# Kernel tuning notes

Hardware: AMD Instinct MI355X
Metric: run time of the kernel (lower is better)

The kernel has to match this reference:

```python
import math
import jax, jax.numpy as jnp
import numpy as np

B, H, D, N, M = 4, 8, 64, 8192, 256
EPS = 1e-6


def sample_orthogonal_random_vectors(num_rows, num_cols, seed=0):
    """Faithful port of FavorAttention.sample_orthogonal_random_vectors."""
    rng = np.random.default_rng(seed)
    num_blocks = math.ceil(num_rows / num_cols)
    unstructured = rng.standard_normal((num_blocks, num_cols, num_cols)).astype(np.float32)
    norm = np.linalg.norm(unstructured, axis=-1).reshape(-1, 1)
    q, _ = np.linalg.qr(unstructured)                 # reduced QR per block
    q = np.transpose(q, (0, 2, 1)).reshape(-1, num_cols)
    q = q[:num_rows, :] * norm[:num_rows, :]
    return jnp.asarray(q, dtype=jnp.float32)


def setup_inputs() -> dict:
    key = jax.random.key(0)
    kq, kk, kv = jax.random.split(key, 3)
    return {
        "query": jax.random.normal(kq, (B, H, D, N), dtype=jnp.float32),
        "key": jax.random.normal(kk, (B, H, D, N), dtype=jnp.float32),
        "value": jax.random.normal(kv, (B, H, D, N), dtype=jnp.float32),
        "projection_matrix": sample_orthogonal_random_vectors(M, D),
    }


def randomized_kernel(x, proj, is_query, eps=EPS):
    """FAVOR+ positive softmax features. x: [B,H,D,N] -> phi: [B,H,M,N]."""
    d = x.shape[2]
    data_normalizer = d ** -0.25
    ratio = proj.shape[0] ** -0.5
    # projected: [B,H,M,N]
    u = jnp.einsum('md,bhdn->bhmn', proj, x) * data_normalizer
    # ||x||^2 / (2*sqrt(d)) per token: [B,H,1,N]
    diag = jnp.sum(x * x, axis=2, keepdims=True) * (data_normalizer ** 2) * 0.5
    if is_query:
        stab = jnp.max(u, axis=2, keepdims=True)            # per-token max over features
    else:
        stab = jnp.max(u, axis=(2, 3), keepdims=True)       # global max per (b,h)
    return ratio * (jnp.exp(u - diag - stab) + eps)


def reference(query, key, value, projection_matrix):
    q_phi = randomized_kernel(query, projection_matrix, is_query=True)    # [B,H,M,N]
    k_phi = randomized_kernel(key, projection_matrix, is_query=False)     # [B,H,M,N]
    # kv = key @ value^T over sequence: [B,H,M,D]
    kv = jnp.einsum('bhmn,bhdn->bhmd', k_phi, value)
    key_norm = jnp.sum(k_phi, axis=3)                                     # [B,H,M]
    out = jnp.einsum('bhmn,bhmd->bhnd', q_phi, kv)                        # [B,H,N,D]
    out_norm = jnp.einsum('bhmn,bhm->bhn', q_phi, key_norm)[..., None]    # [B,H,N,1]
    out = out / out_norm
    return jnp.swapaxes(out, 2, 3)                                        # [B,H,D,N]


if __name__ == '__main__':
    o = reference(**setup_inputs())
    print(o.shape, o.dtype)
```

## Files before the change

### kernel.cpp

```cpp
#include <hip/hip_runtime.h>


typedef short s16x8 __attribute__((ext_vector_type(8)));
typedef float f32x4 __attribute__((ext_vector_type(4)));

#define Dv 64
#define Nv 8192
#define Mv 256
#define BHv 32
#define SPL 16
#define NSPL (Nv / SPL)
#define NCH (NSPL / 64)

#define DNRM 0.3535533905932738f
#define EPSV 1e-6f
#define KSTAB 15.0f

#define OFF_KVA 0
#define OFF_KNA (OFF_KVA + BHv * Mv * Dv)
#define OFF_SVA (OFF_KNA + BHv * Mv)
#define OFF_SGM (OFF_SVA + BHv * Dv)
#define OFF_KNF (OFF_SGM + BHv * 64)
#define OFF_KVT (OFF_KNF + BHv * Mv)
#define ZERO_FLOATS (OFF_SVA + BHv * Dv)

__device__ __forceinline__ unsigned short f2b(float x) {
    return __builtin_bit_cast(unsigned short, (__bf16)x);
}

__device__ __forceinline__ s16x8 load_pfrag(const float* __restrict__ proj, int m,
                                            int kc, int q) {
    const float* p = proj + m * 64 + kc * 32 + q * 8;
    s16x8 r;
#pragma unroll
    for (int j = 0; j < 8; ++j) r[j] = (short)f2b(p[j]);
    return r;
}

__global__ __launch_bounds__(256, 2) void favor_kv(const float* __restrict__ key,
                                                   const float* __restrict__ value,
                                                   const float* __restrict__ proj,
                                                   float* __restrict__ ws) {
    __shared__ __align__(16) unsigned short KT[64][72];
    __shared__ __align__(16) unsigned short VL[64][72];
    __shared__ __align__(16) unsigned short PH[256][40];
    __shared__ __align__(16) float dred[16][64];
    __shared__ __align__(16) float dgl[64];
    const int tid = threadIdx.x;
    const int w = tid >> 6, l = tid & 63, c = l & 15, q = l >> 4;
    const int g = tid >> 4, cs = tid & 15;
    const int s = blockIdx.x, bh = blockIdx.y;
    const float* kp = key + (size_t)bh * Dv * Nv;
    const float* vp = value + (size_t)bh * Dv * Nv;

    s16x8 P[4][2];
#pragma unroll
    for (int mt = 0; mt < 4; ++mt)
#pragma unroll
        for (int kc = 0; kc < 2; ++kc)
            P[mt][kc] = load_pfrag(proj, (4 * w + mt) * 16 + c, kc, q);

    f32x4 kva[4][4];
#pragma unroll
    for (int mt = 0; mt < 4; ++mt)
#pragma unroll
        for (int dt = 0; dt < 4; ++dt) kva[mt][dt] = (f32x4){0.f, 0.f, 0.f, 0.f};
    float kn[4] = {0.f, 0.f, 0.f, 0.f};
    float sv[4] = {0.f, 0.f, 0.f, 0.f};
    float tmax = -3.0e38f;

    for (int ch = 0; ch < NCH; ++ch) {
        const int n0 = s * NSPL + ch * 64;
        if (ch) __syncthreads();
        {
            float4 kk[4], vv[4];
#pragma unroll
            for (int di = 0; di < 4; ++di) {
                kk[di] = *(const float4*)&kp[(4 * g + di) * Nv + n0 + 4 * cs];
                vv[di] = *(const float4*)&vp[(4 * g + di) * Nv + n0 + 4 * cs];
            }
#pragma unroll
            for (int j = 0; j < 4; ++j) {
                const float k0 = ((const float*)&kk[0])[j];
                const float k1 = ((const float*)&kk[1])[j];
                const float k2 = ((const float*)&kk[2])[j];
                const float k3 = ((const float*)&kk[3])[j];
                *(short4*)&KT[4 * cs + j][4 * g] =
                    make_short4((short)f2b(k0), (short)f2b(k1), (short)f2b(k2),
                                (short)f2b(k3));
                dred[g][4 * cs + j] = (k0 * k0 + k1 * k1) + (k2 * k2 + k3 * k3);
            }
#pragma unroll
            for (int di = 0; di < 4; ++di) {
                *(short4*)&VL[4 * g + di][4 * cs] = make_short4(
                    (short)f2b(vv[di].x), (short)f2b(vv[di].y),
                    (short)f2b(vv[di].z), (short)f2b(vv[di].w));
                sv[di] += (vv[di].x + vv[di].y) + (vv[di].z + vv[di].w);
            }
        }
        __syncthreads();
        if (tid < 64) {
            float ds = 0.f;
#pragma unroll
            for (int gg = 0; gg < 16; ++gg) ds += dred[gg][tid];
            dgl[tid] = ds * 0.0625f;
        }
        __syncthreads();
#pragma unroll
        for (int h = 0; h < 2; ++h) {
#pragma unroll
            for (int nt2 = 0; nt2 < 2; ++nt2) {
                const int nt = 2 * h + nt2;
                const s16x8 a0 = *(const s16x8*)&KT[nt * 16 + c][q * 8];
                const s16x8 a1 = *(const s16x8*)&KT[nt * 16 + c][32 + q * 8];
                const float4 dg = *(const float4*)&dgl[nt * 16 + q * 4];
#pragma unroll
                for (int mt = 0; mt < 4; ++mt) {
                    f32x4 u = {0.f, 0.f, 0.f, 0.f};
                    u = __builtin_amdgcn_mfma_f32_16x16x32_bf16(a0, P[mt][0], u, 0, 0, 0);
                    u = __builtin_amdgcn_mfma_f32_16x16x32_bf16(a1, P[mt][1], u, 0, 0, 0);
                    tmax = fmaxf(tmax, fmaxf(fmaxf(u[0], u[1]), fmaxf(u[2], u[3])));
                    const float e0 = __expf(u[0] * DNRM - dg.x - KSTAB);
                    const float e1 = __expf(u[1] * DNRM - dg.y - KSTAB);
                    const float e2 = __expf(u[2] * DNRM - dg.z - KSTAB);
                    const float e3 = __expf(u[3] * DNRM - dg.w - KSTAB);
                    kn[mt] += (e0 + e1) + (e2 + e3);
                    *(short4*)&PH[(4 * w + mt) * 16 + c][nt2 * 16 + q * 4] =
                        make_short4((short)f2b(e0), (short)f2b(e1),
                                    (short)f2b(e2), (short)f2b(e3));
                }
            }
            s16x8 bf[4];
#pragma unroll
            for (int dt = 0; dt < 4; ++dt)
                bf[dt] = *(const s16x8*)&VL[dt * 16 + c][h * 32 + q * 8];
#pragma unroll
            for (int mt = 0; mt < 4; ++mt) {
                const s16x8 a = *(const s16x8*)&PH[(4 * w + mt) * 16 + c][q * 8];
#pragma unroll
                for (int dt = 0; dt < 4; ++dt)
                    kva[mt][dt] = __builtin_amdgcn_mfma_f32_16x16x32_bf16(
                        a, bf[dt], kva[mt][dt], 0, 0, 0);
            }
        }
    }
#pragma unroll
    for (int off = 1; off < 64; off <<= 1)
        tmax = fmaxf(tmax, __shfl_xor(tmax, off, 64));
    if (l == 0) ws[OFF_SGM + bh * 64 + s * 4 + w] = tmax * DNRM;
    float* kvp = ws + OFF_KVA + (size_t)bh * Mv * Dv;
#pragma unroll
    for (int mt = 0; mt < 4; ++mt) {
        const int mrow = (4 * w + mt) * 16 + 4 * q;
#pragma unroll
        for (int dt = 0; dt < 4; ++dt) {
            const int dcol = dt * 16 + c;
#pragma unroll
            for (int r = 0; r < 4; ++r)
                atomicAdd(&kvp[(size_t)(mrow + r) * Dv + dcol], kva[mt][dt][r]);
        }
    }
#pragma unroll
    for (int mt = 0; mt < 4; ++mt) {
        kn[mt] += __shfl_xor(kn[mt], 16, 64);
        kn[mt] += __shfl_xor(kn[mt], 32, 64);
    }
    if (q == 0) {
#pragma unroll
        for (int mt = 0; mt < 4; ++mt)
            atomicAdd(&ws[OFF_KNA + bh * Mv + (4 * w + mt) * 16 + c], kn[mt]);
    }
    __syncthreads();
    float* sp = &dred[0][0];
#pragma unroll
    for (int di = 0; di < 4; ++di) sp[(4 * g + di) * 16 + cs] = sv[di];
    __syncthreads();
    if (tid < 64) {
        float t2 = 0.f;
#pragma unroll
        for (int j = 0; j < 16; ++j) t2 += sp[tid * 16 + j];
        atomicAdd(&ws[OFF_SVA + bh * 64 + tid], t2);
    }
}

__global__ __launch_bounds__(256) void favor_kvred(float* __restrict__ ws) {
    __shared__ float sAl;
    const int t = threadIdx.x, f = blockIdx.x, bh = blockIdx.y;
    if (t < 64) {
        float v = ws[OFF_SGM + bh * 64 + t];
#pragma unroll
        for (int off = 1; off < 64; off <<= 1)
            v = fmaxf(v, __shfl_xor(v, off, 64));
        if (t == 0) sAl = __expf(KSTAB - v);
    }
    __syncthreads();
    const float al = sAl;
    const int flat = f * 4096 + t * 16;
    const int m = flat >> 6, d0 = flat & 63;
    const float* kva = ws + OFF_KVA + (size_t)bh * Mv * Dv;
    const float* sva = ws + OFF_SVA + bh * 64;
    unsigned short* kvT =
        (unsigned short*)(ws + OFF_KVT) + (size_t)bh * 64 * 256;
    float4 vv[4];
#pragma unroll
    for (int i = 0; i < 4; ++i) vv[i] = *(const float4*)&kva[flat + 4 * i];
#pragma unroll
    for (int i = 0; i < 4; ++i) {
#pragma unroll
        for (int j = 0; j < 4; ++j) {
            const int d = d0 + 4 * i + j;
            const float val = ((const float*)&vv[i])[j] * al + EPSV * sva[d];
            kvT[(size_t)d * 256 + m] = f2b(val);
        }
    }
    if (t < 64) {
        const int mm = f * 64 + t;
        ws[OFF_KNF + bh * Mv + mm] =
            ws[OFF_KNA + bh * Mv + mm] * al + EPSV * (float)Nv;
    }
}

__global__ __launch_bounds__(256, 2) void favor_out(const float* __restrict__ query,
                                                    const float* __restrict__ proj,
                                                    const float* __restrict__ ws,
                                                    float* __restrict__ out) {
    __shared__ __align__(16) unsigned short PHT[64][264];
    __shared__ float npart[4][64];
    __shared__ float knl[256];
    __shared__ float cw[4][64];
    __shared__ float stabl[64];
    __shared__ float dql[64];
    unsigned short (*QT)[72] = (unsigned short (*)[72]) & PHT[0][0];
    float (*dred)[64] = (float (*)[64])((char*)&PHT[0][0] + 9216);
    const int tid = threadIdx.x;
    const int w = tid >> 6, l = tid & 63, c = l & 15, q = l >> 4;
    const int g = tid >> 4, cs = tid & 15;
    const int nb = blockIdx.x, bh = blockIdx.y;
    const int n0 = nb * 64;
    const float* qp = query + (size_t)bh * Dv * Nv;
    const unsigned short* kvT =
        (const unsigned short*)(ws + OFF_KVT) + (size_t)bh * 64 * 256;

    {
        float4 qq[4];
#pragma unroll
        for (int di = 0; di < 4; ++di)
            qq[di] = *(const float4*)&qp[(4 * g + di) * Nv + n0 + 4 * cs];
#pragma unroll
        for (int j = 0; j < 4; ++j) {
            const float v0 = ((const float*)&qq[0])[j];
            const float v1 = ((const float*)&qq[1])[j];
            const float v2 = ((const float*)&qq[2])[j];
            const float v3 = ((const float*)&qq[3])[j];
            *(short4*)&QT[4 * cs + j][4 * g] =
                make_short4((short)f2b(v0), (short)f2b(v1), (short)f2b(v2),
                            (short)f2b(v3));
            dred[g][4 * cs + j] = (v0 * v0 + v1 * v1) + (v2 * v2 + v3 * v3);
        }
    }
    knl[tid] = ws[OFF_KNF + bh * Mv + tid];

    s16x8 P[4][2];
#pragma unroll
    for (int mt = 0; mt < 4; ++mt)
#pragma unroll
        for (int kc = 0; kc < 2; ++kc)
            P[mt][kc] = load_pfrag(proj, (4 * w + mt) * 16 + c, kc, q);
    __syncthreads();

    f32x4 u[4][4];
#pragma unroll
    for (int mt = 0; mt < 4; ++mt)
#pragma unroll
        for (int nt = 0; nt < 4; ++nt) u[mt][nt] = (f32x4){0.f, 0.f, 0.f, 0.f};
#pragma unroll
    for (int nt = 0; nt < 4; ++nt) {
        const s16x8 b0 = *(const s16x8*)&QT[nt * 16 + c][q * 8];
        const s16x8 b1 = *(const s16x8*)&QT[nt * 16 + c][32 + q * 8];
#pragma unroll
        for (int mt = 0; mt < 4; ++mt) {
            u[mt][nt] =
                __builtin_amdgcn_mfma_f32_16x16x32_bf16(P[mt][0], b0, u[mt][nt], 0, 0, 0);
            u[mt][nt] =
                __builtin_amdgcn_mfma_f32_16x16x32_bf16(P[mt][1], b1, u[mt][nt], 0, 0, 0);
        }
    }
#pragma unroll
    for (int nt = 0; nt < 4; ++nt) {
        float vm = -3.4e38f;
#pragma unroll
        for (int mt = 0; mt < 4; ++mt)
            vm = fmaxf(vm, fmaxf(fmaxf(u[mt][nt][0], u[mt][nt][1]),
                                 fmaxf(u[mt][nt][2], u[mt][nt][3])));
        vm = fmaxf(vm, __shfl_xor(vm, 16, 64));
        vm = fmaxf(vm, __shfl_xor(vm, 32, 64));
        if (q == 0) cw[w][nt * 16 + c] = vm;
    }
    __syncthreads();
    if (tid < 64) {
        stabl[tid] =
            fmaxf(fmaxf(cw[0][tid], cw[1][tid]), fmaxf(cw[2][tid], cw[3][tid]));
        float dsum = 0.f;
#pragma unroll
        for (int gg = 0; gg < 16; ++gg) dsum += dred[gg][tid];
        dql[tid] = dsum * 0.0625f;
    }
    __syncthreads();
#pragma unroll
    for (int nt = 0; nt < 4; ++nt) {
        const float sr = stabl[nt * 16 + c];
        const float dq = dql[nt * 16 + c];
        float np = 0.f;
#pragma unroll
        for (int mt = 0; mt < 4; ++mt) {
            const float e0 = __expf((u[mt][nt][0] - sr) * DNRM - dq) + EPSV;
            const float e1 = __expf((u[mt][nt][1] - sr) * DNRM - dq) + EPSV;
            const float e2 = __expf((u[mt][nt][2] - sr) * DNRM - dq) + EPSV;
            const float e3 = __expf((u[mt][nt][3] - sr) * DNRM - dq) + EPSV;
            const int mb = (4 * w + mt) * 16 + 4 * q;
            np += e0 * knl[mb] + e1 * knl[mb + 1] + e2 * knl[mb + 2] +
                  e3 * knl[mb + 3];
            *(short4*)&PHT[nt * 16 + c][mb] = make_short4(
                (short)f2b(e0), (short)f2b(e1), (short)f2b(e2), (short)f2b(e3));
        }
        np += __shfl_xor(np, 16, 64);
        np += __shfl_xor(np, 32, 64);
        if (q == 0) npart[w][nt * 16 + c] = np;
    }
    __syncthreads();
    f32x4 acc[4];
#pragma unroll
    for (int dt = 0; dt < 4; ++dt) acc[dt] = (f32x4){0.f, 0.f, 0.f, 0.f};
#pragma unroll
    for (int kc = 0; kc < 8; ++kc) {
        const s16x8 a = *(const s16x8*)&PHT[w * 16 + c][kc * 32 + q * 8];
#pragma unroll
        for (int dt = 0; dt < 4; ++dt) {
            const s16x8 b =
                *(const s16x8*)&kvT[(size_t)(dt * 16 + c) * 256 + kc * 32 + q * 8];
            acc[dt] = __builtin_amdgcn_mfma_f32_16x16x32_bf16(a, b, acc[dt], 0, 0, 0);
        }
    }
    __syncthreads();
    float* ot = (float*)&PHT[0][0];
    float rn[4];
#pragma unroll
    for (int r = 0; r < 4; ++r) {
        const int nl = w * 16 + 4 * q + r;
        rn[r] = 1.0f / ((npart[0][nl] + npart[1][nl]) +
                        (npart[2][nl] + npart[3][nl]));
    }
#pragma unroll
    for (int dt = 0; dt < 4; ++dt)
#pragma unroll
        for (int r = 0; r < 4; ++r)
            ot[(dt * 16 + c) * 68 + (w * 16 + 4 * q + r)] = acc[dt][r] * rn[r];
    __syncthreads();
    float* op = out + (size_t)bh * Dv * Nv;
    {
        const int d = tid >> 2, ng = (tid & 3) * 16;
#pragma unroll
        for (int i = 0; i < 4; ++i) {
            const float4 v = *(const float4*)&ot[d * 68 + ng + i * 4];
            *(float4*)&op[d * Nv + n0 + ng + i * 4] = v;
        }
    }
}

extern "C" void kernel_launch(void* const* d_in, const int* in_sizes, int n_in,
                              void* d_out, int out_size, void* d_ws, size_t ws_size,
                              hipStream_t stream) {
    const float* q = (const float*)d_in[0];
    const float* k = (const float*)d_in[1];
    const float* v = (const float*)d_in[2];
    const float* proj = (const float*)d_in[3];
    float* ws = (float*)d_ws;
    float* out = (float*)d_out;

    hipMemsetAsync(ws, 0, (size_t)ZERO_FLOATS * sizeof(float), stream);
    favor_kv<<<dim3(SPL, 32), 256, 0, stream>>>(k, v, proj, ws);
    favor_kvred<<<dim3(4, 32), 256, 0, stream>>>(ws);
    favor_out<<<dim3(Nv / 64, 32), 256, 0, stream>>>(q, proj, ws, out);
}
```

Measured before the change: 332.5 us.

## Split favor_kv across 8 waves and replace atomics with per-split partial buffers

The key/value phase now runs 512 threads per block. Half the threads load and convert key, the other half value, and each wave handles 2 feature tiles instead of 4. Global atomicAdd accumulation of kv, key norms and value sums is replaced by per-split partial buffers that favor_kvred reduces, which also removes the workspace memset. The stabilizer constant is folded into the diag term so each exponent needs one FMA. In exchange the workspace grows by 16x for the partial kv buffers, and the reduce kernel reads more data.

```diff
diff --git a/kernel.cpp b/kernel.cpp
--- a/kernel.cpp
+++ b/kernel.cpp
@@ -16,13 +16,12 @@
 #define EPSV 1e-6f
 #define KSTAB 15.0f
 
-#define OFF_KVA 0
-#define OFF_KNA (OFF_KVA + BHv * Mv * Dv)
-#define OFF_SVA (OFF_KNA + BHv * Mv)
-#define OFF_SGM (OFF_SVA + BHv * Dv)
-#define OFF_KNF (OFF_SGM + BHv * 64)
-#define OFF_KVT (OFF_KNF + BHv * Mv)
-#define ZERO_FLOATS (OFF_SVA + BHv * Dv)
+#define OFF_SGM 0
+#define OFF_SVP (OFF_SGM + BHv * SPL * 8)
+#define OFF_KNP (OFF_SVP + BHv * SPL * 64)
+#define OFF_KNF (OFF_KNP + BHv * SPL * Mv)
+#define OFF_KVP (OFF_KNF + BHv * Mv)
+#define OFF_KVT (OFF_KVP + BHv * SPL * Mv * Dv)
 
 __device__ __forceinline__ unsigned short f2b(float x) {
     return __builtin_bit_cast(unsigned short, (__bf16)x);
@@ -37,7 +36,7 @@
     return r;
 }
 
-__global__ __launch_bounds__(256, 2) void favor_kv(const float* __restrict__ key,
+__global__ __launch_bounds__(512, 4) void favor_kv(const float* __restrict__ key,
                                                    const float* __restrict__ value,
                                                    const float* __restrict__ proj,
                                                    float* __restrict__ ws) {
@@ -48,37 +47,36 @@
     __shared__ __align__(16) float dgl[64];
     const int tid = threadIdx.x;
     const int w = tid >> 6, l = tid & 63, c = l & 15, q = l >> 4;
-    const int g = tid >> 4, cs = tid & 15;
+    const int sg = tid >> 4, cs = tid & 15;
     const int s = blockIdx.x, bh = blockIdx.y;
     const float* kp = key + (size_t)bh * Dv * Nv;
     const float* vp = value + (size_t)bh * Dv * Nv;
 
-    s16x8 P[4][2];
-#pragma unroll
-    for (int mt = 0; mt < 4; ++mt)
+    s16x8 P[2][2];
+#pragma unroll
+    for (int mt = 0; mt < 2; ++mt)
 #pragma unroll
         for (int kc = 0; kc < 2; ++kc)
-            P[mt][kc] = load_pfrag(proj, (4 * w + mt) * 16 + c, kc, q);
-
-    f32x4 kva[4][4];
-#pragma unroll
-    for (int mt = 0; mt < 4; ++mt)
+            P[mt][kc] = load_pfrag(proj, (2 * w + mt) * 16 + c, kc, q);
+
+    f32x4 kva[2][4];
+#pragma unroll
+    for (int mt = 0; mt < 2; ++mt)
 #pragma unroll
         for (int dt = 0; dt < 4; ++dt) kva[mt][dt] = (f32x4){0.f, 0.f, 0.f, 0.f};
-    float kn[4] = {0.f, 0.f, 0.f, 0.f};
+    float kn[2] = {0.f, 0.f};
     float sv[4] = {0.f, 0.f, 0.f, 0.f};
     float tmax = -3.0e38f;
 
     for (int ch = 0; ch < NCH; ++ch) {
         const int n0 = s * NSPL + ch * 64;
         if (ch) __syncthreads();
-        {
-            float4 kk[4], vv[4];
-#pragma unroll
-            for (int di = 0; di < 4; ++di) {
+        if (sg < 16) {
+            const int g = sg;
+            float4 kk[4];
+#pragma unroll
+            for (int di = 0; di < 4; ++di)
                 kk[di] = *(const float4*)&kp[(4 * g + di) * Nv + n0 + 4 * cs];
-                vv[di] = *(const float4*)&vp[(4 * g + di) * Nv + n0 + 4 * cs];
-            }
 #pragma unroll
             for (int j = 0; j < 4; ++j) {
                 const float k0 = ((const float*)&kk[0])[j];
@@ -90,9 +88,15 @@
                                 (short)f2b(k3));
                 dred[g][4 * cs + j] = (k0 * k0 + k1 * k1) + (k2 * k2 + k3 * k3);
             }
+        } else {
+            const int g2 = sg - 16;
+            float4 vv[4];
+#pragma unroll
+            for (int di = 0; di < 4; ++di)
+                vv[di] = *(const float4*)&vp[(4 * g2 + di) * Nv + n0 + 4 * cs];
 #pragma unroll
             for (int di = 0; di < 4; ++di) {
-                *(short4*)&VL[4 * g + di][4 * cs] = make_short4(
+                *(short4*)&VL[4 * g2 + di][4 * cs] = make_short4(
                     (short)f2b(vv[di].x), (short)f2b(vv[di].y),
                     (short)f2b(vv[di].z), (short)f2b(vv[di].w));
                 sv[di] += (vv[di].x + vv[di].y) + (vv[di].z + vv[di].w);
@@ -103,7 +107,7 @@
             float ds = 0.f;
 #pragma unroll
             for (int gg = 0; gg < 16; ++gg) ds += dred[gg][tid];
-            dgl[tid] = ds * 0.0625f;
+            dgl[tid] = ds * 0.0625f + KSTAB;
         }
         __syncthreads();
 #pragma unroll
@@ -115,17 +119,17 @@
                 const s16x8 a1 = *(const s16x8*)&KT[nt * 16 + c][32 + q * 8];
                 const float4 dg = *(const float4*)&dgl[nt * 16 + q * 4];
 #pragma unroll
-                for (int mt = 0; mt < 4; ++mt) {
+                for (int mt = 0; mt < 2; ++mt) {
                     f32x4 u = {0.f, 0.f, 0.f, 0.f};
                     u = __builtin_amdgcn_mfma_f32_16x16x32_bf16(a0, P[mt][0], u, 0, 0, 0);
                     u = __builtin_amdgcn_mfma_f32_16x16x32_bf16(a1, P[mt][1], u, 0, 0, 0);
                     tmax = fmaxf(tmax, fmaxf(fmaxf(u[0], u[1]), fmaxf(u[2], u[3])));
-                    const float e0 = __expf(u[0] * DNRM - dg.x - KSTAB);
-                    const float e1 = __expf(u[1] * DNRM - dg.y - KSTAB);
-                    const float e2 = __expf(u[2] * DNRM - dg.z - KSTAB);
-                    const float e3 = __expf(u[3] * DNRM - dg.w - KSTAB);
+                    const float e0 = __expf(__builtin_fmaf(u[0], DNRM, -dg.x));
+                    const float e1 = __expf(__builtin_fmaf(u[1], DNRM, -dg.y));
+                    const float e2 = __expf(__builtin_fmaf(u[2], DNRM, -dg.z));
+                    const float e3 = __expf(__builtin_fmaf(u[3], DNRM, -dg.w));
                     kn[mt] += (e0 + e1) + (e2 + e3);
-                    *(short4*)&PH[(4 * w + mt) * 16 + c][nt2 * 16 + q * 4] =
+                    *(short4*)&PH[(2 * w + mt) * 16 + c][nt2 * 16 + q * 4] =
                         make_short4((short)f2b(e0), (short)f2b(e1),
                                     (short)f2b(e2), (short)f2b(e3));
                 }
@@ -135,8 +139,8 @@
             for (int dt = 0; dt < 4; ++dt)
                 bf[dt] = *(const s16x8*)&VL[dt * 16 + c][h * 32 + q * 8];
 #pragma unroll
-            for (int mt = 0; mt < 4; ++mt) {
-                const s16x8 a = *(const s16x8*)&PH[(4 * w + mt) * 16 + c][q * 8];
+            for (int mt = 0; mt < 2; ++mt) {
+                const s16x8 a = *(const s16x8*)&PH[(2 * w + mt) * 16 + c][q * 8];
 #pragma unroll
                 for (int dt = 0; dt < 4; ++dt)
                     kva[mt][dt] = __builtin_amdgcn_mfma_f32_16x16x32_bf16(
@@ -147,76 +151,89 @@
 #pragma unroll
     for (int off = 1; off < 64; off <<= 1)
         tmax = fmaxf(tmax, __shfl_xor(tmax, off, 64));
-    if (l == 0) ws[OFF_SGM + bh * 64 + s * 4 + w] = tmax * DNRM;
-    float* kvp = ws + OFF_KVA + (size_t)bh * Mv * Dv;
-#pragma unroll
-    for (int mt = 0; mt < 4; ++mt) {
-        const int mrow = (4 * w + mt) * 16 + 4 * q;
+    if (l == 0) ws[OFF_SGM + (bh * SPL + s) * 8 + w] = tmax * DNRM;
+    float* kvp = ws + OFF_KVP + (size_t)(bh * SPL + s) * Mv * Dv;
+#pragma unroll
+    for (int mt = 0; mt < 2; ++mt) {
+        const int mrow = (2 * w + mt) * 16 + 4 * q;
 #pragma unroll
         for (int dt = 0; dt < 4; ++dt) {
             const int dcol = dt * 16 + c;
 #pragma unroll
             for (int r = 0; r < 4; ++r)
-                atomicAdd(&kvp[(size_t)(mrow + r) * Dv + dcol], kva[mt][dt][r]);
-        }
-    }
-#pragma unroll
-    for (int mt = 0; mt < 4; ++mt) {
+                kvp[(size_t)(mrow + r) * Dv + dcol] = kva[mt][dt][r];
+        }
+    }
+#pragma unroll
+    for (int mt = 0; mt < 2; ++mt) {
         kn[mt] += __shfl_xor(kn[mt], 16, 64);
         kn[mt] += __shfl_xor(kn[mt], 32, 64);
     }
     if (q == 0) {
-#pragma unroll
-        for (int mt = 0; mt < 4; ++mt)
-            atomicAdd(&ws[OFF_KNA + bh * Mv + (4 * w + mt) * 16 + c], kn[mt]);
+        float* knp = ws + OFF_KNP + (bh * SPL + s) * Mv;
+#pragma unroll
+        for (int mt = 0; mt < 2; ++mt) knp[(2 * w + mt) * 16 + c] = kn[mt];
     }
     __syncthreads();
     float* sp = &dred[0][0];
-#pragma unroll
-    for (int di = 0; di < 4; ++di) sp[(4 * g + di) * 16 + cs] = sv[di];
+    if (sg >= 16) {
+        const int g2 = sg - 16;
+#pragma unroll
+        for (int di = 0; di < 4; ++di) sp[(4 * g2 + di) * 16 + cs] = sv[di];
+    }
     __syncthreads();
     if (tid < 64) {
         float t2 = 0.f;
 #pragma unroll
         for (int j = 0; j < 16; ++j) t2 += sp[tid * 16 + j];
-        atomicAdd(&ws[OFF_SVA + bh * 64 + tid], t2);
+        ws[OFF_SVP + (bh * SPL + s) * 64 + tid] = t2;
     }
 }
 
 __global__ __launch_bounds__(256) void favor_kvred(float* __restrict__ ws) {
     __shared__ float sAl;
+    __shared__ float svl[64];
     const int t = threadIdx.x, f = blockIdx.x, bh = blockIdx.y;
+    const int flat = f * 1024 + t * 4;
+    const int m = flat >> 6, d0 = flat & 63;
     if (t < 64) {
-        float v = ws[OFF_SGM + bh * 64 + t];
+        float v = fmaxf(ws[OFF_SGM + bh * 128 + t],
+                        ws[OFF_SGM + bh * 128 + 64 + t]);
 #pragma unroll
         for (int off = 1; off < 64; off <<= 1)
             v = fmaxf(v, __shfl_xor(v, off, 64));
         if (t == 0) sAl = __expf(KSTAB - v);
+    } else if (t < 128) {
+        const int d = t - 64;
+        float x = 0.f;
+#pragma unroll
+        for (int s2 = 0; s2 < SPL; ++s2)
+            x += ws[OFF_SVP + (bh * SPL + s2) * 64 + d];
+        svl[d] = x;
     }
     __syncthreads();
     const float al = sAl;
-    const int flat = f * 4096 + t * 16;
-    const int m = flat >> 6, d0 = flat & 63;
-    const float* kva = ws + OFF_KVA + (size_t)bh * Mv * Dv;
-    const float* sva = ws + OFF_SVA + bh * 64;
-    unsigned short* kvT =
-        (unsigned short*)(ws + OFF_KVT) + (size_t)bh * 64 * 256;
-    float4 vv[4];
-#pragma unroll
-    for (int i = 0; i < 4; ++i) vv[i] = *(const float4*)&kva[flat + 4 * i];
-#pragma unroll
-    for (int i = 0; i < 4; ++i) {
-#pragma unroll
-        for (int j = 0; j < 4; ++j) {
-            const int d = d0 + 4 * i + j;
-            const float val = ((const float*)&vv[i])[j] * al + EPSV * sva[d];
-            kvT[(size_t)d * 256 + m] = f2b(val);
-        }
-    }
-    if (t < 64) {
-        const int mm = f * 64 + t;
-        ws[OFF_KNF + bh * Mv + mm] =
-            ws[OFF_KNA + bh * Mv + mm] * al + EPSV * (float)Nv;
+    float4 acc = make_float4(0.f, 0.f, 0.f, 0.f);
+    for (int s2 = 0; s2 < SPL; ++s2) {
+        const float4 v =
+            *(const float4*)&ws[OFF_KVP + ((size_t)(bh * SPL + s2) << 14) + flat];
+        acc.x += v.x; acc.y += v.y; acc.z += v.z; acc.w += v.w;
+    }
+    acc.x = acc.x * al + EPSV * svl[d0 + 0];
+    acc.y = acc.y * al + EPSV * svl[d0 + 1];
+    acc.z = acc.z * al + EPSV * svl[d0 + 2];
+    acc.w = acc.w * al + EPSV * svl[d0 + 3];
+    unsigned short* kvT = (unsigned short*)(ws + OFF_KVT);
+    kvT[(bh * 64 + d0 + 0) * 256 + m] = f2b(acc.x);
+    kvT[(bh * 64 + d0 + 1) * 256 + m] = f2b(acc.y);
+    kvT[(bh * 64 + d0 + 2) * 256 + m] = f2b(acc.z);
+    kvT[(bh * 64 + d0 + 3) * 256 + m] = f2b(acc.w);
+    if (t < 16) {
+        const int mm = f * 16 + t;
+        float kk = 0.f;
+        for (int s2 = 0; s2 < SPL; ++s2)
+            kk += ws[OFF_KNP + (bh * SPL + s2) * Mv + mm];
+        ws[OFF_KNF + bh * Mv + mm] = kk * al + EPSV * (float)Nv;
     }
 }
 
@@ -377,8 +394,7 @@
     float* ws = (float*)d_ws;
     float* out = (float*)d_out;
 
-    hipMemsetAsync(ws, 0, (size_t)ZERO_FLOATS * sizeof(float), stream);
-    favor_kv<<<dim3(SPL, 32), 256, 0, stream>>>(k, v, proj, ws);
-    favor_kvred<<<dim3(4, 32), 256, 0, stream>>>(ws);
+    favor_kv<<<dim3(SPL, 32), 512, 0, stream>>>(k, v, proj, ws);
+    favor_kvred<<<dim3(16, 32), 256, 0, stream>>>(ws);
     favor_out<<<dim3(Nv / 64, 32), 256, 0, stream>>>(q, proj, ws, out);
 }
```

Measured after the change: 327.9 us. Within noise of the previous version (-1.4%).
